# Performance work log

Hardware: AMD Instinct MI355X
Metric: run time of the kernel (lower is better)

The kernel has to match this reference:

```python
import jax, jax.numpy as jnp
import numpy as np

D_MODEL = 2048
N_HEADS = 16
N_KV = 4
HEAD_DIM = D_MODEL // N_HEADS  # 128
QK_EPS = 1e-6


def setup_inputs() -> dict:
    key = jax.random.key(0)
    ks = jax.random.split(key, 8)
    B, L = 2, 2048
    x = jax.random.normal(ks[0], (B, L, D_MODEL), dtype=jnp.float32)
    cos = jax.random.uniform(ks[1], (B, L, N_HEADS, HEAD_DIM), dtype=jnp.float32)
    sin = jax.random.uniform(ks[2], (B, L, N_HEADS, HEAD_DIM), dtype=jnp.float32)
    mask = jnp.ones((B, L), dtype=jnp.int32)
    s = 1.0 / np.sqrt(D_MODEL)
    Wq = jax.random.normal(ks[3], (D_MODEL, D_MODEL), dtype=jnp.float32) * s
    Wk = jax.random.normal(ks[4], (D_MODEL, N_KV * HEAD_DIM), dtype=jnp.float32) * s
    Wv = jax.random.normal(ks[5], (D_MODEL, N_KV * HEAD_DIM), dtype=jnp.float32) * s
    Wo = jax.random.normal(ks[6], (D_MODEL, D_MODEL), dtype=jnp.float32) * s
    return {"x": x, "cos": cos, "sin": sin, "mask": mask,
            "Wq": Wq, "Wk": Wk, "Wv": Wv, "Wo": Wo}


def apply_rope(t, cos, sin):
    # t: (..., head_dim); rotate-half style pairing (first half, second half)
    dim = t.shape[-1] // 2
    c, s = cos[..., :dim], sin[..., :dim]
    x1, x2 = t[..., :dim], t[..., dim:]
    return jnp.concatenate([x1 * c - x2 * s, x2 * c + x1 * s], axis=-1)


def _qk_rms(t):
    t32 = t.astype(jnp.float32)
    ms = jnp.mean(jnp.square(t32), axis=-1, keepdims=True)
    return (t32 * jax.lax.rsqrt(ms + QK_EPS)).astype(t.dtype)


def reference(x, cos, sin, mask, Wq, Wk, Wv, Wo):
    B, L, _ = x.shape
    groups = N_HEADS // N_KV
    q = (x @ Wq).reshape(B, L, N_HEADS, HEAD_DIM)
    k = (x @ Wk).reshape(B, L, N_KV, HEAD_DIM)
    v = (x @ Wv).reshape(B, L, N_KV, HEAD_DIM)
    q = apply_rope(q, cos, sin)
    k = apply_rope(k, cos[:, :, :N_KV, :], sin[:, :, :N_KV, :])
    # fp32 QK RMS-norm
    q = _qk_rms(q)
    k = _qk_rms(k)
    # GQA head repeat: (B,L,KV,hd) -> (B,L,H,hd)
    k = jnp.repeat(k, groups, axis=2)
    v = jnp.repeat(v, groups, axis=2)
    scale = 1.0 / jnp.sqrt(jnp.float32(HEAD_DIM))
    scores = jnp.einsum('blhd,bmhd->bhlm', q, k) * scale  # (B,H,L,L)
    large_neg = jnp.asarray(-10000.0, scores.dtype)
    key_mask = mask.astype(scores.dtype).reshape(B, 1, 1, L)
    scores = scores + (1.0 - key_mask) * large_neg
    causal = jnp.tril(jnp.ones((L, L), dtype=scores.dtype)).reshape(1, 1, L, L)
    scores = scores + (1.0 - causal) * large_neg
    attn = jax.nn.softmax(scores.astype(jnp.float32), axis=-1).astype(v.dtype)
    out = jnp.einsum('bhql,blhd->bqhd', attn, v).reshape(B, L, D_MODEL)
    return out @ Wo
```

## Files before the change

kernel.cpp:

```cpp
#include <hip/hip_runtime.h>
#include <hip/hip_bf16.h>

using bf16 = __hip_bfloat16;
using bf16x8 = __attribute__((ext_vector_type(8))) short;
using f32x4 = __attribute__((ext_vector_type(4))) float;

#define MFMA16(a, b, c) __builtin_amdgcn_mfma_f32_16x16x32_bf16((a), (b), (c), 0, 0, 0)

static __device__ __forceinline__ float bf2f(bf16 v) { return __bfloat162float(v); }
static __device__ __forceinline__ bf16 f2bf(float v) { return __float2bfloat16(v); }

typedef const __attribute__((address_space(1))) void* gptr_t;
typedef __attribute__((address_space(3))) void* lptr_t;
static __device__ __forceinline__ void gload16(const void* g, void* l) {
    __builtin_amdgcn_global_load_lds((gptr_t)g, (lptr_t)l, 16, 0, 0);
}

__global__ __launch_bounds__(256) void transpose_w(const float* __restrict__ W,
                                                   bf16* __restrict__ Wt, int N) {
    const int n0 = blockIdx.x * 32;
    const int k0 = blockIdx.y * 32;
    __shared__ __align__(16) float tile[32][36];
    const int t = threadIdx.x;
    {
        const int i = t >> 3, j4 = (t & 7) * 4;
        *reinterpret_cast<float4*>(&tile[i][j4]) =
            *reinterpret_cast<const float4*>(&W[(size_t)(k0 + i) * N + n0 + j4]);
    }
    __syncthreads();
    {
        const int j = t >> 3, i4 = (t & 7) * 4;
        alignas(8) bf16 v4[4];
#pragma unroll
        for (int u = 0; u < 4; ++u) v4[u] = f2bf(tile[i4 + u][j]);
        *reinterpret_cast<uint2*>(&Wt[(size_t)(n0 + j) * 2048 + k0 + i4]) =
            *reinterpret_cast<uint2*>(v4);
    }
}

__global__ __launch_bounds__(256) void convert_x(const float* __restrict__ X,
                                                 bf16* __restrict__ Xb, int n8) {
    int idx = blockIdx.x * 256 + threadIdx.x;
    if (idx >= n8) return;
    const float4 a = reinterpret_cast<const float4*>(X)[idx * 2];
    const float4 c = reinterpret_cast<const float4*>(X)[idx * 2 + 1];
    alignas(16) bf16 v8[8];
    v8[0] = f2bf(a.x); v8[1] = f2bf(a.y); v8[2] = f2bf(a.z); v8[3] = f2bf(a.w);
    v8[4] = f2bf(c.x); v8[5] = f2bf(c.y); v8[6] = f2bf(c.z); v8[7] = f2bf(c.w);
    reinterpret_cast<int4*>(Xb)[idx] = *reinterpret_cast<int4*>(v8);
}

template <typename OUT_T>
__global__ __launch_bounds__(256) void gemm_bt(const bf16* __restrict__ A,
                                               const bf16* __restrict__ Bt,
                                               OUT_T* __restrict__ C,
                                               int M, int N, int K) {
    __shared__ __align__(16) bf16 As[128 * 32];
    __shared__ __align__(16) bf16 Bs[128 * 32];
    const int t = threadIdx.x;
    const int lane = t & 63;
    const int wave = t >> 6;
    const int m0 = blockIdx.y * 128;
    const int n0 = blockIdx.x * 128;
    const int wr = (wave >> 1) * 64;
    const int wc = (wave & 1) * 64;
    const int fr = lane & 15;
    const int fg = lane >> 4;
    f32x4 acc[4][4] = {};
    const int g0 = wave * 2 * 64 + lane;
    const int g1 = g0 + 64;
    const int r0 = g0 >> 2, c0 = (g0 & 3) * 8;
    const int r1 = g1 >> 2, c1 = (g1 & 3) * 8;
    for (int k0 = 0; k0 < K; k0 += 32) {
        __syncthreads();
        gload16(&A[(size_t)(m0 + r0) * K + k0 + c0], &As[(size_t)g0 * 8 - lane * 8]);
        gload16(&A[(size_t)(m0 + r1) * K + k0 + c1], &As[(size_t)g1 * 8 - lane * 8]);
        gload16(&Bt[(size_t)(n0 + r0) * K + k0 + c0], &Bs[(size_t)g0 * 8 - lane * 8]);
        gload16(&Bt[(size_t)(n0 + r1) * K + k0 + c1], &Bs[(size_t)g1 * 8 - lane * 8]);
        __syncthreads();
        bf16x8 af[4], bfv[4];
#pragma unroll
        for (int m = 0; m < 4; ++m)
            af[m] = *reinterpret_cast<const bf16x8*>(&As[(wr + m * 16 + fr) * 32 + fg * 8]);
#pragma unroll
        for (int n = 0; n < 4; ++n)
            bfv[n] = *reinterpret_cast<const bf16x8*>(&Bs[(wc + n * 16 + fr) * 32 + fg * 8]);
#pragma unroll
        for (int m = 0; m < 4; ++m)
#pragma unroll
            for (int n = 0; n < 4; ++n)
                acc[m][n] = MFMA16(af[m], bfv[n], acc[m][n]);
    }
#pragma unroll
    for (int m = 0; m < 4; ++m) {
#pragma unroll
        for (int r = 0; r < 4; ++r) {
            const int grow = m0 + wr + m * 16 + fg * 4 + r;
#pragma unroll
            for (int n = 0; n < 4; ++n) {
                const int gcol = n0 + wc + n * 16 + fr;
                const float v = acc[m][n][r];
                if constexpr (sizeof(OUT_T) == 2)
                    C[(size_t)grow * N + gcol] = f2bf(v);
                else
                    C[(size_t)grow * N + gcol] = v;
            }
        }
    }
}

__global__ __launch_bounds__(256) void rope_rms(const bf16* __restrict__ qkv,
                                                const float* __restrict__ cosb,
                                                const float* __restrict__ sinb,
                                                bf16* __restrict__ Qo,
                                                bf16* __restrict__ Ko) {
    const int row = blockIdx.x;
    const int b = row >> 11, l = row & 2047;
    const int wave = threadIdx.x >> 6, lane = threadIdx.x & 63;
    const bf16* src = qkv + (size_t)row * 3072;
#pragma unroll
    for (int i = 0; i < 4; ++i) {
        const int hh = wave * 4 + i;
        float x1 = bf2f(src[hh * 128 + lane]);
        float x2 = bf2f(src[hh * 128 + 64 + lane]);
        size_t cs = ((size_t)row * 16 + hh) * 128 + lane;
        float c = cosb[cs], sn = sinb[cs];
        float o1 = x1 * c - x2 * sn;
        float o2 = x2 * c + x1 * sn;
        float ss = o1 * o1 + o2 * o2;
#pragma unroll
        for (int off = 32; off >= 1; off >>= 1) ss += __shfl_xor(ss, off);
        float scf = rsqrtf(ss * (1.0f / 128.0f) + 1e-6f);
        bf16* dst = Qo + ((size_t)(b * 16 + hh) * 2048 + l) * 128;
        dst[lane] = f2bf(o1 * scf);
        dst[64 + lane] = f2bf(o2 * scf);
    }
    {
        const int hv = wave;
        float x1 = bf2f(src[2048 + hv * 128 + lane]);
        float x2 = bf2f(src[2048 + hv * 128 + 64 + lane]);
        size_t cs = ((size_t)row * 16 + hv) * 128 + lane;
        float c = cosb[cs], sn = sinb[cs];
        float o1 = x1 * c - x2 * sn;
        float o2 = x2 * c + x1 * sn;
        float ss = o1 * o1 + o2 * o2;
#pragma unroll
        for (int off = 32; off >= 1; off >>= 1) ss += __shfl_xor(ss, off);
        float scf = rsqrtf(ss * (1.0f / 128.0f) + 1e-6f);
        bf16* dst = Ko + ((size_t)(b * 4 + hv) * 2048 + l) * 128;
        dst[lane] = f2bf(o1 * scf);
        dst[64 + lane] = f2bf(o2 * scf);
    }
}

__global__ __launch_bounds__(256) void transpose_v(const bf16* __restrict__ qkv,
                                                   bf16* __restrict__ Vt) {
    const int bk = blockIdx.x;
    const int l0 = blockIdx.y * 32;
    const int d0 = blockIdx.z * 32;
    const int b = bk >> 2, kv = bk & 3;
    __shared__ __align__(16) bf16 tile[32][40];
    const int t = threadIdx.x;
    {
        const int i = t >> 3, j4 = (t & 7) * 4;
        *reinterpret_cast<uint2*>(&tile[i][j4]) =
            *reinterpret_cast<const uint2*>(
                &qkv[(size_t)(b * 2048 + l0 + i) * 3072 + 2560 + kv * 128 + d0 + j4]);
    }
    __syncthreads();
    {
        const int j = t >> 3, i4 = (t & 7) * 4;
        alignas(8) bf16 v4[4];
#pragma unroll
        for (int u = 0; u < 4; ++u) v4[u] = tile[i4 + u][j];
        *reinterpret_cast<uint2*>(&Vt[((size_t)bk * 128 + d0 + j) * 2048 + l0 + i4]) =
            *reinterpret_cast<uint2*>(v4);
    }
}

__global__ __launch_bounds__(256, 4) void attn_fwd(const bf16* __restrict__ Q,
                                                   const bf16* __restrict__ Kb,
                                                   const bf16* __restrict__ Vt,
                                                   const int* __restrict__ maskp,
                                                   bf16* __restrict__ O) {
    const int bid = (blockIdx.x & 7) * 128 + (blockIdx.x >> 3);
    const int qt = bid & 31;
    const int h = (bid >> 5) & 15;
    const int b = bid >> 9;
    const int wave = threadIdx.x >> 6;
    const int lane = threadIdx.x & 63;
    const int fr = lane & 15, fg = lane >> 4;
    const int q0 = qt * 64 + wave * 16;
    const int hk = h >> 2;
    __shared__ __align__(16) bf16 Ks[2][32 * 128];
    __shared__ __align__(16) bf16 Vs[2][128 * 32];
    __shared__ __align__(16) bf16 P[4][16][40];
    const bf16* qp = Q + (size_t)(b * 16 + h) * 2048 * 128;
    const bf16* kp = Kb + (size_t)(b * 4 + hk) * 2048 * 128;
    const bf16* vp = Vt + (size_t)(b * 4 + hk) * 128 * 2048;
    const int* mp = maskp + b * 2048;

    bf16x8 qf[4];
#pragma unroll
    for (int ks = 0; ks < 4; ++ks)
        qf[ks] = *reinterpret_cast<const bf16x8*>(
            &qp[(size_t)(q0 + fr) * 128 + ks * 32 + fg * 8]);

    f32x4 acc[8] = {};
    float mrow[4] = {-1e30f, -1e30f, -1e30f, -1e30f};
    float lrow[4] = {0.f, 0.f, 0.f, 0.f};
    const float SCALE = 0.08838834764831845f;
    const int nkv = 2 * qt + 2;

    const int gk0 = wave * 2 * 64 + lane, gk1 = gk0 + 64;
    const int kr0 = gk0 >> 4, kc0 = (gk0 & 15) ^ (kr0 & 7);
    const int kr1 = gk1 >> 4, kc1 = (gk1 & 15) ^ (kr1 & 7);
    const int vr0 = gk0 >> 2, vc0 = (gk0 & 3) ^ (vr0 & 3);
    const int vr1 = gk1 >> 2, vc1 = (gk1 & 3) ^ (vr1 & 3);
    const int kdst0 = (wave * 2) * 512, kdst1 = kdst0 + 512;

#define STAGE_KV(buf, kv0)                                                        \
    do {                                                                          \
        gload16(&kp[(size_t)((kv0) + kr0) * 128 + kc0 * 8], &Ks[buf][kdst0]);     \
        gload16(&kp[(size_t)((kv0) + kr1) * 128 + kc1 * 8], &Ks[buf][kdst1]);     \
        gload16(&vp[(size_t)vr0 * 2048 + (kv0) + vc0 * 8], &Vs[buf][kdst0]);      \
        gload16(&vp[(size_t)vr1 * 2048 + (kv0) + vc1 * 8], &Vs[buf][kdst1]);      \
    } while (0)

    STAGE_KV(0, 0);
    __syncthreads();
    int cur = 0;

    for (int t = 0; t < nkv; ++t) {
        const int kv0 = t * 32;
        if (t + 1 < nkv) STAGE_KV(cur ^ 1, kv0 + 32);
        if (kv0 <= q0 + 15) {
            const char* kbase = (const char*)&Ks[cur][0];
            const char* vbase = (const char*)&Vs[cur][0];
            f32x4 s[2] = {};
            __builtin_amdgcn_s_setprio(1);
#pragma unroll
            for (int st = 0; st < 2; ++st) {
                const int krow = st * 16 + fr;
#pragma unroll
                for (int ks = 0; ks < 4; ++ks) {
                    bf16x8 kf = *reinterpret_cast<const bf16x8*>(
                        kbase + krow * 256 + (((ks * 64 + fg * 16)) ^ ((fr & 7) << 4)));
                    s[st] = MFMA16(qf[ks], kf, s[st]);
                }
            }
            __builtin_amdgcn_s_setprio(0);
            float scl[4];
#pragma unroll
            for (int st = 0; st < 2; ++st) {
                const int col = kv0 + st * 16 + fr;
                const float madd = -10000.0f * (float)(1 - mp[col]);
#pragma unroll
                for (int r = 0; r < 4; ++r) {
                    const int row = q0 + fg * 4 + r;
                    float v = s[st][r] * SCALE + madd;
                    if (col > row) v -= 10000.0f;
                    s[st][r] = v;
                }
            }
#pragma unroll
            for (int r = 0; r < 4; ++r) {
                float mx = fmaxf(s[0][r], s[1][r]);
                mx = fmaxf(mx, __shfl_xor(mx, 1));
                mx = fmaxf(mx, __shfl_xor(mx, 2));
                mx = fmaxf(mx, __shfl_xor(mx, 4));
                mx = fmaxf(mx, __shfl_xor(mx, 8));
                float nm = fmaxf(mrow[r], mx);
                float sc = __expf(mrow[r] - nm);
                mrow[r] = nm;
                scl[r] = sc;
                float p0 = __expf(s[0][r] - nm);
                float p1 = __expf(s[1][r] - nm);
                s[0][r] = p0;
                s[1][r] = p1;
                float rs = p0 + p1;
                rs += __shfl_xor(rs, 1);
                rs += __shfl_xor(rs, 2);
                rs += __shfl_xor(rs, 4);
                rs += __shfl_xor(rs, 8);
                lrow[r] = lrow[r] * sc + rs;
            }
#pragma unroll
            for (int st = 0; st < 2; ++st)
#pragma unroll
                for (int r = 0; r < 4; ++r)
                    P[wave][fg * 4 + r][st * 16 + fr] = f2bf(s[st][r]);
#pragma unroll
            for (int n = 0; n < 8; ++n) {
                acc[n][0] *= scl[0];
                acc[n][1] *= scl[1];
                acc[n][2] *= scl[2];
                acc[n][3] *= scl[3];
            }
            bf16x8 pf = *reinterpret_cast<const bf16x8*>(&P[wave][fr][fg * 8]);
            __builtin_amdgcn_s_setprio(1);
#pragma unroll
            for (int n = 0; n < 8; ++n) {
                const int vrow = n * 16 + fr;
                bf16x8 vf = *reinterpret_cast<const bf16x8*>(
                    vbase + vrow * 64 + ((fg * 16) ^ ((fr & 3) << 4)));
                acc[n] = MFMA16(pf, vf, acc[n]);
            }
            __builtin_amdgcn_s_setprio(0);
        }
        __syncthreads();
        cur ^= 1;
    }
#undef STAGE_KV

    float inv[4];
#pragma unroll
    for (int r = 0; r < 4; ++r) inv[r] = 1.0f / lrow[r];
#pragma unroll
    for (int n = 0; n < 8; ++n) {
#pragma unroll
        for (int r = 0; r < 4; ++r) {
            const float v = acc[n][r] * inv[r];
            O[(size_t)(b * 2048 + q0 + fg * 4 + r) * 2048 + h * 128 + n * 16 + fr] =
                f2bf(v);
        }
    }
}

extern "C" void kernel_launch(void* const* d_in, const int* in_sizes, int n_in,
                              void* d_out, int out_size, void* d_ws, size_t ws_size,
                              hipStream_t stream) {
    const float* x = (const float*)d_in[0];
    const float* cosb = (const float*)d_in[1];
    const float* sinb = (const float*)d_in[2];
    const int* mask = (const int*)d_in[3];
    const float* Wq = (const float*)d_in[4];
    const float* Wk = (const float*)d_in[5];
    const float* Wv = (const float*)d_in[6];
    const float* Wo = (const float*)d_in[7];
    float* out = (float*)d_out;

    char* p = (char*)d_ws;
    bf16* wqkv_t = (bf16*)p; p += (size_t)3072 * 2048 * 2;
    bf16* wo_t  = (bf16*)p; p += (size_t)2048 * 2048 * 2;
    bf16* x_bf  = (bf16*)p; p += (size_t)4096 * 2048 * 2;
    bf16* qkv_bf = (bf16*)p; p += (size_t)4096 * 3072 * 2;
    bf16* q_bf  = (bf16*)p; p += (size_t)2 * 16 * 2048 * 128 * 2;
    bf16* k_bf  = (bf16*)p; p += (size_t)2 * 4 * 2048 * 128 * 2;
    bf16* v_t   = (bf16*)p; p += (size_t)2 * 4 * 128 * 2048 * 2;
    bf16* o_bf  = x_bf;

    transpose_w<<<dim3(64, 64), 256, 0, stream>>>(Wq, wqkv_t, 2048);
    transpose_w<<<dim3(16, 64), 256, 0, stream>>>(Wk, wqkv_t + (size_t)2048 * 2048, 512);
    transpose_w<<<dim3(16, 64), 256, 0, stream>>>(Wv, wqkv_t + (size_t)2560 * 2048, 512);
    transpose_w<<<dim3(64, 64), 256, 0, stream>>>(Wo, wo_t, 2048);
    convert_x<<<4096, 256, 0, stream>>>(x, x_bf, 4096 * 2048 / 8);
    gemm_bt<bf16><<<dim3(24, 32), 256, 0, stream>>>(x_bf, wqkv_t, qkv_bf, 4096, 3072, 2048);
    rope_rms<<<4096, 256, 0, stream>>>(qkv_bf, cosb, sinb, q_bf, k_bf);
    transpose_v<<<dim3(8, 64, 4), 256, 0, stream>>>(qkv_bf, v_t);
    attn_fwd<<<1024, 256, 0, stream>>>(q_bf, k_bf, v_t, mask, o_bf);
    gemm_bt<float><<<dim3(16, 32), 256, 0, stream>>>(o_bf, wo_t, out, 4096, 2048, 2048);
}
```

Baseline: 497.0 us.

## Lazy softmax rescale, fragment-order LDS layout, reversed causal tile order in attention

The attention kernel now skips the running-max update and accumulator rescale whenever the new block max stays within a threshold of 8 of the running max. This removes an exp and 32 multiplies per row in most iterations, and stays exact because the final normalization divides by the matching sum. K and V tiles are staged into LDS already in MFMA fragment order, so each lane reads a contiguous 16 bytes without XOR swizzle address math. Query tiles are scheduled longest-first to reduce causal tail imbalance, and the key mask is precomputed once as a float additive bias by a small new kernel. The unswizzled layout may cause bank conflicts on the async LDS writes, and the lazy rescale allows unnormalized values up to e^8 before bf16 conversion.

Result: slower. 521.4 us (+4.9%).

```diff
diff --git a/kernel.cpp b/kernel.cpp
--- a/kernel.cpp
+++ b/kernel.cpp
@@ -48,6 +48,12 @@
     v8[0] = f2bf(a.x); v8[1] = f2bf(a.y); v8[2] = f2bf(a.z); v8[3] = f2bf(a.w);
     v8[4] = f2bf(c.x); v8[5] = f2bf(c.y); v8[6] = f2bf(c.z); v8[7] = f2bf(c.w);
     reinterpret_cast<int4*>(Xb)[idx] = *reinterpret_cast<int4*>(v8);
+}
+
+__global__ __launch_bounds__(256) void mask_to_f(const int* __restrict__ m,
+                                                 float* __restrict__ f, int n) {
+    int i = blockIdx.x * 256 + threadIdx.x;
+    if (i < n) f[i] = -10000.0f * (float)(1 - m[i]);
 }
 
 template <typename OUT_T>
@@ -181,10 +187,10 @@
 __global__ __launch_bounds__(256, 4) void attn_fwd(const bf16* __restrict__ Q,
                                                    const bf16* __restrict__ Kb,
                                                    const bf16* __restrict__ Vt,
-                                                   const int* __restrict__ maskp,
+                                                   const float* __restrict__ maddf,
                                                    bf16* __restrict__ O) {
     const int bid = (blockIdx.x & 7) * 128 + (blockIdx.x >> 3);
-    const int qt = bid & 31;
+    const int qt = 31 - (bid & 31);
     const int h = (bid >> 5) & 15;
     const int b = bid >> 9;
     const int wave = threadIdx.x >> 6;
@@ -192,13 +198,13 @@
     const int fr = lane & 15, fg = lane >> 4;
     const int q0 = qt * 64 + wave * 16;
     const int hk = h >> 2;
-    __shared__ __align__(16) bf16 Ks[2][32 * 128];
-    __shared__ __align__(16) bf16 Vs[2][128 * 32];
+    __shared__ __align__(16) bf16 Ks[2][4096];
+    __shared__ __align__(16) bf16 Vs[2][4096];
     __shared__ __align__(16) bf16 P[4][16][40];
     const bf16* qp = Q + (size_t)(b * 16 + h) * 2048 * 128;
     const bf16* kp = Kb + (size_t)(b * 4 + hk) * 2048 * 128;
     const bf16* vp = Vt + (size_t)(b * 4 + hk) * 128 * 2048;
-    const int* mp = maskp + b * 2048;
+    const float* mp = maddf + b * 2048;
 
     bf16x8 qf[4];
 #pragma unroll
@@ -212,19 +218,20 @@
     const float SCALE = 0.08838834764831845f;
     const int nkv = 2 * qt + 2;
 
-    const int gk0 = wave * 2 * 64 + lane, gk1 = gk0 + 64;
-    const int kr0 = gk0 >> 4, kc0 = (gk0 & 15) ^ (kr0 & 7);
-    const int kr1 = gk1 >> 4, kc1 = (gk1 & 15) ^ (kr1 & 7);
-    const int vr0 = gk0 >> 2, vc0 = (gk0 & 3) ^ (vr0 & 3);
-    const int vr1 = gk1 >> 2, vc1 = (gk1 & 3) ^ (vr1 & 3);
-    const int kdst0 = (wave * 2) * 512, kdst1 = kdst0 + 512;
-
-#define STAGE_KV(buf, kv0)                                                        \
-    do {                                                                          \
-        gload16(&kp[(size_t)((kv0) + kr0) * 128 + kc0 * 8], &Ks[buf][kdst0]);     \
-        gload16(&kp[(size_t)((kv0) + kr1) * 128 + kc1 * 8], &Ks[buf][kdst1]);     \
-        gload16(&vp[(size_t)vr0 * 2048 + (kv0) + vc0 * 8], &Vs[buf][kdst0]);      \
-        gload16(&vp[(size_t)vr1 * 2048 + (kv0) + vc1 * 8], &Vs[buf][kdst1]);      \
+    const int c0 = wave, c1 = wave + 4;
+    const int krow0 = lane & 15;
+    const int krow1 = 16 + (lane & 15);
+    const int kcol = wave * 32 + (lane >> 4) * 8;
+    const int vrow0 = wave * 16 + (lane & 15);
+    const int vrow1 = vrow0 + 64;
+    const int vcol = (lane >> 4) * 8;
+
+#define STAGE_KV(buf, kv0)                                                     \
+    do {                                                                       \
+        gload16(&kp[(size_t)((kv0) + krow0) * 128 + kcol], &Ks[buf][c0 * 512]);\
+        gload16(&kp[(size_t)((kv0) + krow1) * 128 + kcol], &Ks[buf][c1 * 512]);\
+        gload16(&vp[(size_t)vrow0 * 2048 + (kv0) + vcol], &Vs[buf][c0 * 512]); \
+        gload16(&vp[(size_t)vrow1 * 2048 + (kv0) + vcol], &Vs[buf][c1 * 512]); \
     } while (0)
 
     STAGE_KV(0, 0);
@@ -235,26 +242,21 @@
         const int kv0 = t * 32;
         if (t + 1 < nkv) STAGE_KV(cur ^ 1, kv0 + 32);
         if (kv0 <= q0 + 15) {
-            const char* kbase = (const char*)&Ks[cur][0];
-            const char* vbase = (const char*)&Vs[cur][0];
             f32x4 s[2] = {};
             __builtin_amdgcn_s_setprio(1);
 #pragma unroll
-            for (int st = 0; st < 2; ++st) {
-                const int krow = st * 16 + fr;
+            for (int st = 0; st < 2; ++st)
 #pragma unroll
                 for (int ks = 0; ks < 4; ++ks) {
                     bf16x8 kf = *reinterpret_cast<const bf16x8*>(
-                        kbase + krow * 256 + (((ks * 64 + fg * 16)) ^ ((fr & 7) << 4)));
+                        &Ks[cur][((st * 4 + ks) * 64 + lane) * 8]);
                     s[st] = MFMA16(qf[ks], kf, s[st]);
                 }
-            }
             __builtin_amdgcn_s_setprio(0);
-            float scl[4];
 #pragma unroll
             for (int st = 0; st < 2; ++st) {
                 const int col = kv0 + st * 16 + fr;
-                const float madd = -10000.0f * (float)(1 - mp[col]);
+                const float madd = mp[col];
 #pragma unroll
                 for (int r = 0; r < 4; ++r) {
                     const int row = q0 + fg * 4 + r;
@@ -263,47 +265,63 @@
                     s[st][r] = v;
                 }
             }
+            float mx[4];
 #pragma unroll
             for (int r = 0; r < 4; ++r) {
-                float mx = fmaxf(s[0][r], s[1][r]);
-                mx = fmaxf(mx, __shfl_xor(mx, 1));
-                mx = fmaxf(mx, __shfl_xor(mx, 2));
-                mx = fmaxf(mx, __shfl_xor(mx, 4));
-                mx = fmaxf(mx, __shfl_xor(mx, 8));
-                float nm = fmaxf(mrow[r], mx);
-                float sc = __expf(mrow[r] - nm);
-                mrow[r] = nm;
-                scl[r] = sc;
-                float p0 = __expf(s[0][r] - nm);
-                float p1 = __expf(s[1][r] - nm);
-                s[0][r] = p0;
-                s[1][r] = p1;
-                float rs = p0 + p1;
-                rs += __shfl_xor(rs, 1);
-                rs += __shfl_xor(rs, 2);
-                rs += __shfl_xor(rs, 4);
-                rs += __shfl_xor(rs, 8);
-                lrow[r] = lrow[r] * sc + rs;
+                float m0 = fmaxf(s[0][r], s[1][r]);
+                m0 = fmaxf(m0, __shfl_xor(m0, 1));
+                m0 = fmaxf(m0, __shfl_xor(m0, 2));
+                m0 = fmaxf(m0, __shfl_xor(m0, 4));
+                m0 = fmaxf(m0, __shfl_xor(m0, 8));
+                mx[r] = m0;
+            }
+            const int ok = (mx[0] <= mrow[0] + 8.0f) & (mx[1] <= mrow[1] + 8.0f) &
+                           (mx[2] <= mrow[2] + 8.0f) & (mx[3] <= mrow[3] + 8.0f);
+            if (__all(ok)) {
+#pragma unroll
+                for (int r = 0; r < 4; ++r) {
+                    float p0 = __expf(s[0][r] - mrow[r]);
+                    float p1 = __expf(s[1][r] - mrow[r]);
+                    s[0][r] = p0;
+                    s[1][r] = p1;
+                    float rs = p0 + p1;
+                    rs += __shfl_xor(rs, 1);
+                    rs += __shfl_xor(rs, 2);
+                    rs += __shfl_xor(rs, 4);
+                    rs += __shfl_xor(rs, 8);
+                    lrow[r] += rs;
+                }
+            } else {
+#pragma unroll
+                for (int r = 0; r < 4; ++r) {
+                    float nm = fmaxf(mrow[r], mx[r]);
+                    float sc = __expf(mrow[r] - nm);
+                    float p0 = __expf(s[0][r] - nm);
+                    float p1 = __expf(s[1][r] - nm);
+                    s[0][r] = p0;
+                    s[1][r] = p1;
+                    float rs = p0 + p1;
+                    rs += __shfl_xor(rs, 1);
+                    rs += __shfl_xor(rs, 2);
+                    rs += __shfl_xor(rs, 4);
+                    rs += __shfl_xor(rs, 8);
+                    lrow[r] = lrow[r] * sc + rs;
+                    mrow[r] = nm;
+#pragma unroll
+                    for (int n = 0; n < 8; ++n) acc[n][r] *= sc;
+                }
             }
 #pragma unroll
             for (int st = 0; st < 2; ++st)
 #pragma unroll
                 for (int r = 0; r < 4; ++r)
                     P[wave][fg * 4 + r][st * 16 + fr] = f2bf(s[st][r]);
-#pragma unroll
-            for (int n = 0; n < 8; ++n) {
-                acc[n][0] *= scl[0];
-                acc[n][1] *= scl[1];
-                acc[n][2] *= scl[2];
-                acc[n][3] *= scl[3];
-            }
             bf16x8 pf = *reinterpret_cast<const bf16x8*>(&P[wave][fr][fg * 8]);
             __builtin_amdgcn_s_setprio(1);
 #pragma unroll
             for (int n = 0; n < 8; ++n) {
-                const int vrow = n * 16 + fr;
                 bf16x8 vf = *reinterpret_cast<const bf16x8*>(
-                    vbase + vrow * 64 + ((fg * 16) ^ ((fr & 3) << 4)));
+                    &Vs[cur][(n * 64 + lane) * 8]);
                 acc[n] = MFMA16(pf, vf, acc[n]);
             }
             __builtin_amdgcn_s_setprio(0);
@@ -348,6 +366,7 @@
     bf16* q_bf  = (bf16*)p; p += (size_t)2 * 16 * 2048 * 128 * 2;
     bf16* k_bf  = (bf16*)p; p += (size_t)2 * 4 * 2048 * 128 * 2;
     bf16* v_t   = (bf16*)p; p += (size_t)2 * 4 * 128 * 2048 * 2;
+    float* maddf = (float*)p; p += (size_t)4096 * 4;
     bf16* o_bf  = x_bf;
 
     transpose_w<<<dim3(64, 64), 256, 0, stream>>>(Wq, wqkv_t, 2048);
@@ -355,9 +374,10 @@
     transpose_w<<<dim3(16, 64), 256, 0, stream>>>(Wv, wqkv_t + (size_t)2560 * 2048, 512);
     transpose_w<<<dim3(64, 64), 256, 0, stream>>>(Wo, wo_t, 2048);
     convert_x<<<4096, 256, 0, stream>>>(x, x_bf, 4096 * 2048 / 8);
+    mask_to_f<<<16, 256, 0, stream>>>(mask, maddf, 4096);
     gemm_bt<bf16><<<dim3(24, 32), 256, 0, stream>>>(x_bf, wqkv_t, qkv_bf, 4096, 3072, 2048);
     rope_rms<<<4096, 256, 0, stream>>>(qkv_bf, cosb, sinb, q_bf, k_bf);
     transpose_v<<<dim3(8, 64, 4), 256, 0, stream>>>(qkv_bf, v_t);
-    attn_fwd<<<1024, 256, 0, stream>>>(q_bf, k_bf, v_t, mask, o_bf);
+    attn_fwd<<<1024, 256, 0, stream>>>(q_bf, k_bf, v_t, maddf, o_bf);
     gemm_bt<float><<<dim3(16, 32), 256, 0, stream>>>(o_bf, wo_t, out, 4096, 2048, 2048);
 }
```
